# Kernel optimization log

Measured on AMD Instinct MI355X. Metric: run time of the kernel, lower is better.

## Reference

```python
import jax, jax.numpy as jnp
import numpy as np

B, S, H, D = 2, 2048, 16, 128

def setup_inputs() -> dict:
    key = jax.random.key(0)
    kq, kk, kv = jax.random.split(key, 3)
    q = jax.random.normal(kq, (B, S, H, D), dtype=jnp.float32)
    k = jax.random.normal(kk, (B, S, H, D), dtype=jnp.float32)
    v = jax.random.normal(kv, (B, S, H, D), dtype=jnp.float32)
    return {"q": q, "k": k, "v": v}

def reference(q, k, v):
    # Flash-attention semantics: layout [B, S, H, D], causal mask,
    # softmax_scale = 1/sqrt(head_dim), no dropout/window/alibi/bias.
    scale = 1.0 / jnp.sqrt(jnp.asarray(q.shape[-1], dtype=q.dtype))
    # scores: [B, H, Sq, Sk]
    scores = jnp.einsum("bqhd,bkhd->bhqk", q, k) * scale
    sq, sk = q.shape[1], k.shape[1]
    causal_mask = jnp.arange(sk)[None, :] <= jnp.arange(sq)[:, None]  # [Sq, Sk]
    scores = jnp.where(causal_mask[None, None, :, :], scores, jnp.finfo(scores.dtype).min)
    probs = jax.nn.softmax(scores, axis=-1)
    out = jnp.einsum("bhqk,bkhd->bqhd", probs, v)
    return out
```

## Files before the change

kernel.cpp:

```cpp
#include <hip/hip_runtime.h>
#include <hip/hip_bf16.h>

namespace {

constexpr int Bn = 2, Sn = 2048, Hn = 16, Dn = 128;
constexpr int QBLK = 128;
constexpr int KVBLK = 32;
constexpr int RS = Hn * Dn;
constexpr float QSCALE = 0.08838834764831845f * 1.4426950408889634f;

constexpr size_t IMG_BYTES = (size_t)Bn * Hn * 64 * 8192;
constexpr size_t WS_NEED   = 2 * IMG_BYTES;

typedef __bf16 bf16x8 __attribute__((ext_vector_type(8)));
typedef __bf16 bf16x4 __attribute__((ext_vector_type(4)));
typedef float  f32x16 __attribute__((ext_vector_type(16)));

__device__ __forceinline__ f32x16 mfma32(bf16x8 a, bf16x8 b, f32x16 c) {
  return __builtin_amdgcn_mfma_f32_32x32x16_bf16(a, b, c, 0, 0, 0);
}
__device__ __forceinline__ unsigned pack2(float a, float b) {
  union { __bf16 h[2]; unsigned u; } r;
  r.h[0] = (__bf16)a; r.h[1] = (__bf16)b;
  return r.u;
}
__device__ __forceinline__ float pair_max(float x, int hi) {
  auto r = __builtin_amdgcn_permlane32_swap(__float_as_uint(x), __float_as_uint(x), false, false);
  const float sw = __uint_as_float(hi ? r[0] : r[1]);
  return fmaxf(x, sw);
}
__device__ __forceinline__ float pair_sum(float x, int hi) {
  auto r = __builtin_amdgcn_permlane32_swap(__float_as_uint(x), __float_as_uint(x), false, false);
  const float sw = __uint_as_float(hi ? r[0] : r[1]);
  return x + sw;
}
__device__ __forceinline__ float f4e(const float4& v, int j) {
  return j == 0 ? v.x : j == 1 ? v.y : j == 2 ? v.z : v.w;
}
__device__ __forceinline__ float lane_bcast(int row, float v) {
  return __uint_as_float(__builtin_amdgcn_ds_bpermute(row * 4, __float_as_uint(v)));
}

__device__ __forceinline__ void cp16(const char* g, char* l) {
  __builtin_amdgcn_global_load_lds(
      (const __attribute__((address_space(1))) void*)g,
      (__attribute__((address_space(3))) void*)l, 16, 0, 0);
}

__device__ __forceinline__ void dma_barrier() {
  __builtin_amdgcn_sched_barrier(0);
  asm volatile("s_waitcnt vmcnt(0) lgkmcnt(0)" ::: "memory");
  __builtin_amdgcn_s_barrier();
  __builtin_amdgcn_sched_barrier(0);
}
__device__ __forceinline__ void pipeline_barrier() {
  __builtin_amdgcn_sched_barrier(0);
  asm volatile("s_waitcnt lgkmcnt(0)" ::: "memory");
  __builtin_amdgcn_s_barrier();
  __builtin_amdgcn_sched_barrier(0);
}

__global__ __launch_bounds__(256)
void prep_kv(const float* __restrict__ K, const float* __restrict__ V,
             __bf16* __restrict__ KI, __bf16* __restrict__ VI)
{
  const int gid  = (int)blockIdx.x * 256 + (int)threadIdx.x;
  const int half = gid >> 20;
  const int id   = gid & ((1 << 20) - 1);
  const int chunk = id >> 9;
  const int rem   = id & 511;
  const int bh = chunk >> 6, c = chunk & 63;
  const int b = bh >> 4, h = bh & 15;
  if (half == 0) {
    const int key = rem >> 4, dblk = rem & 15;
    const float* src = K + ((size_t)b * Sn + (size_t)c * 32 + key) * RS + h * Dn + dblk * 8;
    float4 a  = *(const float4*)src;
    float4 c2 = *(const float4*)(src + 4);
    bf16x8 f;
    f[0] = (__bf16)a.x;  f[1] = (__bf16)a.y;  f[2] = (__bf16)a.z;  f[3] = (__bf16)a.w;
    f[4] = (__bf16)c2.x; f[5] = (__bf16)c2.y; f[6] = (__bf16)c2.z; f[7] = (__bf16)c2.w;
    char* dst = (char*)KI + (size_t)chunk * 8192 + ((key * 256 + dblk * 16) ^ ((key & 7) << 4));
    *(bf16x8*)dst = f;
  } else {
    const int d = rem >> 2, koct = rem & 3;
    const float* src = V + ((size_t)b * Sn + (size_t)c * 32 + koct * 8) * RS + h * Dn + d;
    bf16x8 f;
#pragma unroll
    for (int j = 0; j < 8; ++j) f[j] = (__bf16)src[(size_t)j * RS];
    const int off = (d * 64 + koct * 16) ^ ((d & 3) << 4) ^ (((d >> 3) & 1) << 6);
    *(bf16x8*)((char*)VI + (size_t)chunk * 8192 + off) = f;
  }
}

__global__ __launch_bounds__(512)
void fa_fwd_dma(const float* __restrict__ Q, const __bf16* __restrict__ KI,
                const __bf16* __restrict__ VI, float* __restrict__ O)
{
  __shared__ __align__(16) __bf16 Klds[4][4096];
  __shared__ __align__(16) __bf16 Vt[4][4096];

  const int tid  = threadIdx.x;
  const int lane = tid & 63;
  const int wave = tid >> 6;
  const int col  = lane & 31;
  const int hi   = lane >> 5;
  const int grp  = wave >> 2;
  const int wq   = wave & 3;

  const int xcd  = (int)blockIdx.x & 7;
  const int s    = (int)blockIdx.x >> 3;
  const int hidx = xcd * 4 + (s & 3);
  const int b    = hidx >> 4, h = hidx & 15;
  const int s2   = s >> 2;
  const int qt   = (s < 32) ? (15 - s2) : (s2 - 8);
  const int q0w  = qt * QBLK + wq * 32;
  const int T    = 2 * (qt + 1);
  const size_t base = ((size_t)b * Sn) * RS + (size_t)h * Dn;

  const char* KIc = (const char*)KI + (size_t)hidx * 64 * 8192;
  const char* VIc = (const char*)VI + (size_t)hidx * 64 * 8192;

  const int sr = wave >> 1;
  const int hb = (wave & 1) * 4096;
  auto stageK2 = [&](int ss) {
    if (sr < 2) {
      const int ck = 2 * ss + sr;
      const char* g = KIc + (size_t)ck * 8192 + hb;
      char* l = (char*)&Klds[ck & 3][0] + hb;
#pragma unroll
      for (int i = 0; i < 4; ++i) cp16(g + i * 1024 + lane * 16, l + i * 1024);
    }
  };
  auto stageV2 = [&](int ss) {
    if (sr >= 2) {
      const int cv = 2 * ss + (sr - 2);
      const char* g = VIc + (size_t)cv * 8192 + hb;
      char* l = (char*)&Vt[cv & 3][0] + hb;
#pragma unroll
      for (int i = 0; i < 4; ++i) cp16(g + i * 1024 + lane * 16, l + i * 1024);
    }
  };

  const int cswz = (col & 7) << 4;
  const int vswz = ((col & 3) << 4) ^ (((col >> 3) & 1) << 6);

  bf16x8 qf[8];
  {
    const float* qp = Q + base + (size_t)(q0w + col) * RS + hi * 8;
#pragma unroll
    for (int kk = 0; kk < 8; ++kk) {
      float4 a = *(const float4*)(qp + kk * 16);
      float4 c2 = *(const float4*)(qp + kk * 16 + 4);
      bf16x8 f;
      f[0] = (__bf16)(a.x * QSCALE);  f[1] = (__bf16)(a.y * QSCALE);
      f[2] = (__bf16)(a.z * QSCALE);  f[3] = (__bf16)(a.w * QSCALE);
      f[4] = (__bf16)(c2.x * QSCALE); f[5] = (__bf16)(c2.y * QSCALE);
      f[6] = (__bf16)(c2.z * QSCALE); f[7] = (__bf16)(c2.w * QSCALE);
      qf[kk] = f;
    }
  }

  f32x16 o0 = {}, o1 = {}, o2 = {}, o3 = {};
  float m = -1e30f, l = 0.f;

  stageK2(0);
  stageV2(0);
  stageK2(1);
  dma_barrier();

  f32x16 st_cur = {};
  if (grp * KVBLK <= q0w + 31) {
    const char* kb = (const char*)&Klds[grp][0];
    __builtin_amdgcn_s_setprio(1);
#pragma unroll
    for (int kk = 0; kk < 8; ++kk) {
      bf16x8 ka = *(const bf16x8*)(kb + ((col * 256 + kk * 32 + hi * 16) ^ cswz));
      st_cur = mfma32(ka, qf[kk], st_cur);
    }
    __builtin_amdgcn_s_setprio(0);
  }
  dma_barrier();

#pragma unroll 1
  for (int t = 0; t < T; ++t) {
    if (t + 2 < T) stageK2(t + 2);
    if (t + 1 < T) stageV2(t + 1);

    f32x16 stn = {};
    const int icn = 2 * (t + 1) + grp;
    if (t + 1 < T && icn * KVBLK <= q0w + 31) {
      const char* kb = (const char*)&Klds[icn & 3][0];
      __builtin_amdgcn_s_setprio(1);
#pragma unroll
      for (int kk = 0; kk < 8; ++kk) {
        bf16x8 ka = *(const bf16x8*)(kb + ((col * 256 + kk * 32 + hi * 16) ^ cswz));
        stn = mfma32(ka, qf[kk], stn);
      }
      __builtin_amdgcn_s_setprio(0);
    }

    const int kv0 = (2 * t + grp) * KVBLK;
    if (kv0 <= q0w + 31) {
      if (kv0 + KVBLK - 1 > q0w) {
        const int qk = q0w + col - kv0;
#pragma unroll
        for (int r = 0; r < 16; ++r) {
          const int krow = (r & 3) + 8 * (r >> 2) + 4 * hi;
          st_cur[r] = (krow <= qk) ? st_cur[r] : -1e30f;
        }
      }

      float t8[8];
#pragma unroll
      for (int r = 0; r < 8; ++r) t8[r] = fmaxf(st_cur[r], st_cur[r + 8]);
#pragma unroll
      for (int r = 0; r < 4; ++r) t8[r] = fmaxf(t8[r], t8[r + 4]);
      const float pmax = pair_max(fmaxf(fmaxf(t8[0], t8[1]), fmaxf(t8[2], t8[3])), hi);

      if (!__all(pmax <= m + 11.0f)) {
        const float mnew = fmaxf(m, pmax);
        const float al = __builtin_amdgcn_exp2f(m - mnew);
        m = mnew;
        l *= al;
#pragma unroll
        for (int r = 0; r < 16; ++r) {
          const int row = (r & 3) + 8 * (r >> 2) + 4 * hi;
          const float ar = lane_bcast(row, al);
          o0[r] *= ar; o1[r] *= ar; o2[r] *= ar; o3[r] *= ar;
        }
      }

      float s4[4] = {0.f, 0.f, 0.f, 0.f};
#pragma unroll
      for (int r = 0; r < 16; ++r) {
        st_cur[r] = __builtin_amdgcn_exp2f(st_cur[r] - m);
        s4[r & 3] += st_cur[r];
      }
      l += pair_sum((s4[0] + s4[1]) + (s4[2] + s4[3]), hi);

      unsigned cw[8];
#pragma unroll
      for (int i = 0; i < 8; ++i) cw[i] = pack2(st_cur[2 * i], st_cur[2 * i + 1]);
      union { unsigned u[4]; bf16x8 v; } pa0, pa1;
      {
        auto s02 = __builtin_amdgcn_permlane32_swap(cw[0], cw[2], false, false);
        auto s13 = __builtin_amdgcn_permlane32_swap(cw[1], cw[3], false, false);
        auto s46 = __builtin_amdgcn_permlane32_swap(cw[4], cw[6], false, false);
        auto s57 = __builtin_amdgcn_permlane32_swap(cw[5], cw[7], false, false);
        pa0.u[0] = s02[0]; pa0.u[2] = s02[1];
        pa0.u[1] = s13[0]; pa0.u[3] = s13[1];
        pa1.u[0] = s46[0]; pa1.u[2] = s46[1];
        pa1.u[1] = s57[0]; pa1.u[3] = s57[1];
      }

      const char* vb = (const char*)&Vt[(2 * t + grp) & 3][0];
      __builtin_amdgcn_s_setprio(1);
#pragma unroll
      for (int ks = 0; ks < 2; ++ks) {
        const bf16x8 pa = ks ? pa1.v : pa0.v;
#define PV_STEP(ovar, dt) { \
        bf16x8 vf = *(const bf16x8*)(vb + ((((dt)*32 + col) * 64 + ks * 32 + hi * 16) ^ vswz)); \
        ovar = mfma32(pa, vf, ovar); }
        PV_STEP(o0, 0) PV_STEP(o1, 1) PV_STEP(o2, 2) PV_STEP(o3, 3)
#undef PV_STEP
      }
      __builtin_amdgcn_s_setprio(0);
    }
    dma_barrier();
    st_cur = stn;
  }

  float* ob  = reinterpret_cast<float*>(&Klds[0][0]);
  float* mlb = reinterpret_cast<float*>(&Vt[0][0]);
  if (grp == 1) {
    mlb[wq * 128 + lane] = m;
    mlb[wq * 128 + 64 + lane] = l;
#pragma unroll
    for (int r = 0; r < 16; ++r) {
      ob[wq * 1024 + r * 64 + lane] = o0[r];
      ob[4096 + wq * 1024 + r * 64 + lane] = o1[r];
    }
  }
  __syncthreads();
  float f0 = 1.f, f1 = 0.f;
  if (grp == 0) {
    const float m1 = mlb[wq * 128 + lane];
    const float l1 = mlb[wq * 128 + 64 + lane];
    const float mS = fmaxf(m, m1);
    f0 = __builtin_amdgcn_exp2f(m - mS);
    f1 = __builtin_amdgcn_exp2f(m1 - mS);
    l = l * f0 + l1 * f1;
#pragma unroll
    for (int r = 0; r < 16; ++r) {
      const int row = (r & 3) + 8 * (r >> 2) + 4 * hi;
      const float a0 = lane_bcast(row, f0), a1 = lane_bcast(row, f1);
      o0[r] = o0[r] * a0 + ob[wq * 1024 + r * 64 + lane] * a1;
      o1[r] = o1[r] * a0 + ob[4096 + wq * 1024 + r * 64 + lane] * a1;
    }
  }
  __syncthreads();
  if (grp == 1) {
#pragma unroll
    for (int r = 0; r < 16; ++r) {
      ob[wq * 1024 + r * 64 + lane] = o2[r];
      ob[4096 + wq * 1024 + r * 64 + lane] = o3[r];
    }
  }
  __syncthreads();
  if (grp == 0) {
#pragma unroll
    for (int r = 0; r < 16; ++r) {
      const int row = (r & 3) + 8 * (r >> 2) + 4 * hi;
      const float a0 = lane_bcast(row, f0), a1 = lane_bcast(row, f1);
      o2[r] = o2[r] * a0 + ob[wq * 1024 + r * 64 + lane] * a1;
      o3[r] = o3[r] * a0 + ob[4096 + wq * 1024 + r * 64 + lane] * a1;
    }
    const float linv = 1.0f / l;
#pragma unroll
    for (int r = 0; r < 16; ++r) {
      const int row = (r & 3) + 8 * (r >> 2) + 4 * hi;
      const float lr = lane_bcast(row, linv);
      float* op = O + base + (size_t)(q0w + row) * RS + col;
      op[0]  = o0[r] * lr;
      op[32] = o1[r] * lr;
      op[64] = o2[r] * lr;
      op[96] = o3[r] * lr;
    }
  }
}

__global__ __launch_bounds__(512)
void fa_fwd_reg(const float* __restrict__ Q, const float* __restrict__ K,
                const float* __restrict__ V, float* __restrict__ O)
{
  __shared__ __align__(16) __bf16 Klds[6][KVBLK * 128];
  __shared__ __align__(16) __bf16 Vt[4][128 * KVBLK];

  const int tid  = threadIdx.x;
  const int lane = tid & 63;
  const int wave = tid >> 6;
  const int col  = lane & 31;
  const int hi   = lane >> 5;
  const int grp  = wave >> 2;
  const int wq   = wave & 3;

  const int xcd  = (int)blockIdx.x & 7;
  const int s    = (int)blockIdx.x >> 3;
  const int hidx = xcd * 4 + (s & 3);
  const int b    = hidx >> 4, h = hidx & 15;
  const int s2   = s >> 2;
  const int qt   = (s < 32) ? (15 - s2) : (s2 - 8);
  const int q0w  = qt * QBLK + wq * 32;
  const int T    = 2 * (qt + 1);
  const size_t base = ((size_t)b * Sn) * RS + (size_t)h * Dn;

  const int sthalf = tid >> 8, ht = tid & 255;
  const int skey = ht >> 3, sd = (ht & 7) * 16;
  const int vkey4 = (ht & 7) * 4, vd4 = (ht >> 3) * 4;

  float4 kr[4], vr[4];
  auto loadK = [&](int ss) {
    const int kv0 = (2 * ss + sthalf) * KVBLK;
    const float* kp = K + base + (size_t)(kv0 + skey) * RS + sd;
#pragma unroll
    for (int i = 0; i < 4; ++i) kr[i] = *(const float4*)(kp + 4 * i);
  };
  auto loadV = [&](int ss) {
    const int kv0 = (2 * ss + sthalf) * KVBLK;
    const float* vp = V + base + (size_t)(kv0 + vkey4) * RS + vd4;
#pragma unroll
    for (int i = 0; i < 4; ++i) vr[i] = *(const float4*)(vp + (size_t)i * RS);
  };
  auto stageK = [&](int ss) {
    char* kb = (char*)&Klds[(2 * ss + sthalf) % 6][0];
    const int kbase = skey * 256 + sd * 2;
    const int kswz  = (skey & 7) << 4;
#pragma unroll
    for (int i = 0; i < 2; ++i) {
      bf16x8 f;
      f[0] = (__bf16)kr[2*i].x;   f[1] = (__bf16)kr[2*i].y;
      f[2] = (__bf16)kr[2*i].z;   f[3] = (__bf16)kr[2*i].w;
      f[4] = (__bf16)kr[2*i+1].x; f[5] = (__bf16)kr[2*i+1].y;
      f[6] = (__bf16)kr[2*i+1].z; f[7] = (__bf16)kr[2*i+1].w;
      *(bf16x8*)(kb + ((kbase + 16 * i) ^ kswz)) = f;
    }
  };
  auto stageV = [&](int ss) {
    char* vb = (char*)&Vt[(2 * ss + sthalf) & 3][0];
    const int b6 = ((vd4 >> 3) & 1) << 6;
#pragma unroll
    for (int j = 0; j < 4; ++j) {
      bf16x4 w;
      w[0] = (__bf16)f4e(vr[0], j);
      w[1] = (__bf16)f4e(vr[1], j);
      w[2] = (__bf16)f4e(vr[2], j);
      w[3] = (__bf16)f4e(vr[3], j);
      const int addr = (((vd4 + j) * 64 + vkey4 * 2) ^ (j << 4)) ^ b6;
      *(bf16x4*)(vb + addr) = w;
    }
  };

  const int cswz = (col & 7) << 4;
  const int vswz = ((col & 3) << 4) ^ (((col >> 3) & 1) << 6);

  bf16x8 qf[8];
  {
    const float* qp = Q + base + (size_t)(q0w + col) * RS + hi * 8;
#pragma unroll
    for (int kk = 0; kk < 8; ++kk) {
      float4 a = *(const float4*)(qp + kk * 16);
      float4 c2 = *(const float4*)(qp + kk * 16 + 4);
      bf16x8 f;
      f[0] = (__bf16)(a.x * QSCALE);  f[1] = (__bf16)(a.y * QSCALE);
      f[2] = (__bf16)(a.z * QSCALE);  f[3] = (__bf16)(a.w * QSCALE);
      f[4] = (__bf16)(c2.x * QSCALE); f[5] = (__bf16)(c2.y * QSCALE);
      f[6] = (__bf16)(c2.z * QSCALE); f[7] = (__bf16)(c2.w * QSCALE);
      qf[kk] = f;
    }
  }

  f32x16 o0 = {}, o1 = {}, o2 = {}, o3 = {};
  float m = -1e30f, l = 0.f;

  loadK(0); loadV(0);
  stageK(0);
  loadK(1);
  stageV(0);
  loadV(1);
  stageK(1);
  if (2 < T) loadK(2);
  pipeline_barrier();

  f32x16 st_cur = {};
  if (grp * KVBLK <= q0w + 31) {
    const char* kb = (const char*)&Klds[grp][0];
    __builtin_amdgcn_s_setprio(1);
#pragma unroll
    for (int kk = 0; kk < 8; ++kk) {
      bf16x8 ka = *(const bf16x8*)(kb + ((col * 256 + kk * 32 + hi * 16) ^ cswz));
      st_cur = mfma32(ka, qf[kk], st_cur);
    }
    __builtin_amdgcn_s_setprio(0);
  }

#pragma unroll 1
  for (int t = 0; t < T; ++t) {
    f32x16 stn = {};
    const int icn = 2 * (t + 1) + grp;
    if (t + 1 < T && icn * KVBLK <= q0w + 31) {
      const char* kb = (const char*)&Klds[icn % 6][0];
      __builtin_amdgcn_s_setprio(1);
#pragma unroll
      for (int kk = 0; kk < 8; ++kk) {
        bf16x8 ka = *(const bf16x8*)(kb + ((col * 256 + kk * 32 + hi * 16) ^ cswz));
        stn = mfma32(ka, qf[kk], stn);
      }
      __builtin_amdgcn_s_setprio(0);
    }

    if (t + 2 < T) stageK(t + 2);
    if (t + 1 < T) stageV(t + 1);
    if (t + 3 < T) loadK(t + 3);
    if (t + 2 < T) loadV(t + 2);

    const int kv0 = (2 * t + grp) * KVBLK;
    if (kv0 <= q0w + 31) {
      if (kv0 + KVBLK - 1 > q0w) {
        const int qk = q0w + col - kv0;
#pragma unroll
        for (int r = 0; r < 16; ++r) {
          const int krow = (r & 3) + 8 * (r >> 2) + 4 * hi;
          st_cur[r] = (krow <= qk) ? st_cur[r] : -1e30f;
        }
      }

      float t8[8];
#pragma unroll
      for (int r = 0; r < 8; ++r) t8[r] = fmaxf(st_cur[r], st_cur[r + 8]);
#pragma unroll
      for (int r = 0; r < 4; ++r) t8[r] = fmaxf(t8[r], t8[r + 4]);
      const float pmax = pair_max(fmaxf(fmaxf(t8[0], t8[1]), fmaxf(t8[2], t8[3])), hi);

      if (!__all(pmax <= m + 11.0f)) {
        const float mnew = fmaxf(m, pmax);
        const float al = __builtin_amdgcn_exp2f(m - mnew);
        m = mnew;
        l *= al;
#pragma unroll
        for (int r = 0; r < 16; ++r) {
          const int row = (r & 3) + 8 * (r >> 2) + 4 * hi;
          const float ar = lane_bcast(row, al);
          o0[r] *= ar; o1[r] *= ar; o2[r] *= ar; o3[r] *= ar;
        }
      }

      float s4[4] = {0.f, 0.f, 0.f, 0.f};
#pragma unroll
      for (int r = 0; r < 16; ++r) {
        st_cur[r] = __builtin_amdgcn_exp2f(st_cur[r] - m);
        s4[r & 3] += st_cur[r];
      }
      l += pair_sum((s4[0] + s4[1]) + (s4[2] + s4[3]), hi);

      unsigned cw[8];
#pragma unroll
      for (int i = 0; i < 8; ++i) cw[i] = pack2(st_cur[2 * i], st_cur[2 * i + 1]);
      union { unsigned u[4]; bf16x8 v; } pa0, pa1;
      {
        auto s02 = __builtin_amdgcn_permlane32_swap(cw[0], cw[2], false, false);
        auto s13 = __builtin_amdgcn_permlane32_swap(cw[1], cw[3], false, false);
        auto s46 = __builtin_amdgcn_permlane32_swap(cw[4], cw[6], false, false);
        auto s57 = __builtin_amdgcn_permlane32_swap(cw[5], cw[7], false, false);
        pa0.u[0] = s02[0]; pa0.u[2] = s02[1];
        pa0.u[1] = s13[0]; pa0.u[3] = s13[1];
        pa1.u[0] = s46[0]; pa1.u[2] = s46[1];
        pa1.u[1] = s57[0]; pa1.u[3] = s57[1];
      }

      const char* vb = (const char*)&Vt[(2 * t + grp) & 3][0];
      __builtin_amdgcn_s_setprio(1);
#pragma unroll
      for (int ks = 0; ks < 2; ++ks) {
        const bf16x8 pa = ks ? pa1.v : pa0.v;
#define PV_STEP(ovar, dt) { \
        bf16x8 vf = *(const bf16x8*)(vb + ((((dt)*32 + col) * 64 + ks * 32 + hi * 16) ^ vswz)); \
        ovar = mfma32(pa, vf, ovar); }
        PV_STEP(o0, 0) PV_STEP(o1, 1) PV_STEP(o2, 2) PV_STEP(o3, 3)
#undef PV_STEP
      }
      __builtin_amdgcn_s_setprio(0);
    }
    pipeline_barrier();
    st_cur = stn;
  }

  float* ob  = reinterpret_cast<float*>(&Klds[0][0]);
  float* mlb = reinterpret_cast<float*>(&Vt[0][0]);
  if (grp == 1) {
    mlb[wq * 128 + lane] = m;
    mlb[wq * 128 + 64 + lane] = l;
#pragma unroll
    for (int r = 0; r < 16; ++r) {
      ob[wq * 1024 + r * 64 + lane] = o0[r];
      ob[4096 + wq * 1024 + r * 64 + lane] = o1[r];
    }
  }
  __syncthreads();
  float f0 = 1.f, f1 = 0.f;
  if (grp == 0) {
    const float m1 = mlb[wq * 128 + lane];
    const float l1 = mlb[wq * 128 + 64 + lane];
    const float mS = fmaxf(m, m1);
    f0 = __builtin_amdgcn_exp2f(m - mS);
    f1 = __builtin_amdgcn_exp2f(m1 - mS);
    l = l * f0 + l1 * f1;
#pragma unroll
    for (int r = 0; r < 16; ++r) {
      const int row = (r & 3) + 8 * (r >> 2) + 4 * hi;
      const float a0 = lane_bcast(row, f0), a1 = lane_bcast(row, f1);
      o0[r] = o0[r] * a0 + ob[wq * 1024 + r * 64 + lane] * a1;
      o1[r] = o1[r] * a0 + ob[4096 + wq * 1024 + r * 64 + lane] * a1;
    }
  }
  __syncthreads();
  if (grp == 1) {
#pragma unroll
    for (int r = 0; r < 16; ++r) {
      ob[wq * 1024 + r * 64 + lane] = o2[r];
      ob[4096 + wq * 1024 + r * 64 + lane] = o3[r];
    }
  }
  __syncthreads();
  if (grp == 0) {
#pragma unroll
    for (int r = 0; r < 16; ++r) {
      const int row = (r & 3) + 8 * (r >> 2) + 4 * hi;
      const float a0 = lane_bcast(row, f0), a1 = lane_bcast(row, f1);
      o2[r] = o2[r] * a0 + ob[wq * 1024 + r * 64 + lane] * a1;
      o3[r] = o3[r] * a0 + ob[4096 + wq * 1024 + r * 64 + lane] * a1;
    }
    const float linv = 1.0f / l;
#pragma unroll
    for (int r = 0; r < 16; ++r) {
      const int row = (r & 3) + 8 * (r >> 2) + 4 * hi;
      const float lr = lane_bcast(row, linv);
      float* op = O + base + (size_t)(q0w + row) * RS + col;
      op[0]  = o0[r] * lr;
      op[32] = o1[r] * lr;
      op[64] = o2[r] * lr;
      op[96] = o3[r] * lr;
    }
  }
}

}

extern "C" void kernel_launch(void* const* d_in, const int* , int ,
                              void* d_out, int , void* d_ws, size_t ws_size,
                              hipStream_t stream) {
  const float* q = (const float*)d_in[0];
  const float* k = (const float*)d_in[1];
  const float* v = (const float*)d_in[2];
  float* o = (float*)d_out;
  if (d_ws != nullptr && ws_size >= WS_NEED) {
    __bf16* ki = (__bf16*)d_ws;
    __bf16* vi = (__bf16*)((char*)d_ws + IMG_BYTES);
    hipLaunchKernelGGL(prep_kv, dim3(8192), dim3(256), 0, stream, k, v, ki, vi);
    hipLaunchKernelGGL(fa_fwd_dma, dim3(512), dim3(512), 0, stream, q, ki, vi, o);
  } else {
    hipLaunchKernelGGL(fa_fwd_reg, dim3(512), dim3(512), 0, stream, q, k, v, o);
  }
}
```

Measured before the change: 102.3 us.

## Pair causal q-tiles per block and widen KV steps to 64 keys

Each block now handles two complementary query tiles (15-p and p) in sequence, halving the grid to 256 blocks so causal work is balanced per block. Each wave group now processes two 32-key chunks per iteration using an 8-deep LDS ring for K and V, which halves the number of barriers per key. The cost is double the shared memory (128 KB) and more live score registers, which may reduce occupancy. It also serialises two tiles inside one block, so there is less parallelism across CUs.

```diff
diff --git a/kernel.cpp b/kernel.cpp
--- a/kernel.cpp
+++ b/kernel.cpp
@@ -96,8 +96,295 @@
 void fa_fwd_dma(const float* __restrict__ Q, const __bf16* __restrict__ KI,
                 const __bf16* __restrict__ VI, float* __restrict__ O)
 {
-  __shared__ __align__(16) __bf16 Klds[4][4096];
-  __shared__ __align__(16) __bf16 Vt[4][4096];
+  __shared__ __align__(16) __bf16 Klds[8][4096];
+  __shared__ __align__(16) __bf16 Vt[8][4096];
+
+  const int tid  = threadIdx.x;
+  const int lane = tid & 63;
+  const int wave = tid >> 6;
+  const int col  = lane & 31;
+  const int hi   = lane >> 5;
+  const int grp  = wave >> 2;
+  const int wq   = wave & 3;
+
+  const int xcd  = (int)blockIdx.x & 7;
+  const int s    = (int)blockIdx.x >> 3;
+  const int hidx = xcd * 4 + (s & 3);
+  const int b    = hidx >> 4, h = hidx & 15;
+  const int p    = s >> 2;
+  const size_t base = ((size_t)b * Sn) * RS + (size_t)h * Dn;
+
+  const char* KIc = (const char*)KI + (size_t)hidx * 64 * 8192;
+  const char* VIc = (const char*)VI + (size_t)hidx * 64 * 8192;
+
+  auto stageKc = [&](int cc) {
+    const char* g = KIc + (size_t)cc * 8192 + lane * 16;
+    char* l = (char*)&Klds[cc & 7][0];
+#pragma unroll
+    for (int i = 0; i < 8; ++i) cp16(g + i * 1024, l + i * 1024);
+  };
+  auto stageVc = [&](int cc) {
+    const char* g = VIc + (size_t)cc * 8192 + lane * 16;
+    char* l = (char*)&Vt[cc & 7][0];
+#pragma unroll
+    for (int i = 0; i < 8; ++i) cp16(g + i * 1024, l + i * 1024);
+  };
+
+  const int cswz = (col & 7) << 4;
+  const int vswz = ((col & 3) << 4) ^ (((col >> 3) & 1) << 6);
+
+#define QK8(kbp, acc) { \
+  __builtin_amdgcn_s_setprio(1); \
+  _Pragma("unroll") \
+  for (int kk = 0; kk < 8; ++kk) { \
+    bf16x8 ka = *(const bf16x8*)((kbp) + ((col * 256 + kk * 32 + hi * 16) ^ cswz)); \
+    acc = mfma32(ka, qf[kk], acc); \
+  } \
+  __builtin_amdgcn_s_setprio(0); }
+
+#pragma unroll 1
+  for (int tp = 0; tp < 2; ++tp) {
+    const int qt  = tp ? p : (15 - p);
+    const int q0w = qt * QBLK + wq * 32;
+    const int T   = qt + 1;
+
+    bf16x8 qf[8];
+    {
+      const float* qp = Q + base + (size_t)(q0w + col) * RS + hi * 8;
+#pragma unroll
+      for (int kk = 0; kk < 8; ++kk) {
+        float4 a = *(const float4*)(qp + kk * 16);
+        float4 c2 = *(const float4*)(qp + kk * 16 + 4);
+        bf16x8 f;
+        f[0] = (__bf16)(a.x * QSCALE);  f[1] = (__bf16)(a.y * QSCALE);
+        f[2] = (__bf16)(a.z * QSCALE);  f[3] = (__bf16)(a.w * QSCALE);
+        f[4] = (__bf16)(c2.x * QSCALE); f[5] = (__bf16)(c2.y * QSCALE);
+        f[6] = (__bf16)(c2.z * QSCALE); f[7] = (__bf16)(c2.w * QSCALE);
+        qf[kk] = f;
+      }
+    }
+
+    f32x16 o0 = {}, o1 = {}, o2 = {}, o3 = {};
+    float m = -1e30f, l = 0.f;
+
+    if (wave < 4) stageKc(wave); else stageVc(wave - 4);
+    if (T > 1 && wave < 4) stageKc(4 + wave);
+    dma_barrier();
+
+    f32x16 sc0 = {}, sc1 = {};
+    {
+      const int cc = 2 * grp;
+      if (cc * 32 <= q0w + 31) {
+        const char* kb = (const char*)&Klds[cc][0];
+        QK8(kb, sc0)
+        if ((cc + 1) * 32 <= q0w + 31) {
+          const char* kb1 = (const char*)&Klds[cc + 1][0];
+          QK8(kb1, sc1)
+        }
+      }
+    }
+    dma_barrier();
+
+#pragma unroll 1
+    for (int t = 0; t < T; ++t) {
+      if (t + 2 < T && wave < 4) stageKc(4 * (t + 2) + wave);
+      if (t + 1 < T && wave >= 4) stageVc(4 * (t + 1) + (wave - 4));
+
+      f32x16 sn0 = {}, sn1 = {};
+      if (t + 1 < T) {
+        const int cc = 4 * (t + 1) + 2 * grp;
+        if (cc * 32 <= q0w + 31) {
+          const char* kb = (const char*)&Klds[cc & 7][0];
+          QK8(kb, sn0)
+          if ((cc + 1) * 32 <= q0w + 31) {
+            const char* kb1 = (const char*)&Klds[(cc + 1) & 7][0];
+            QK8(kb1, sn1)
+          }
+        }
+      }
+
+      const int cc0 = 4 * t + 2 * grp;
+      const int kv0 = cc0 * 32;
+      if (kv0 <= q0w + 31) {
+        const bool v1 = (kv0 + 32) <= q0w + 31;
+
+        if (kv0 + 31 > q0w) {
+          const int qk = q0w + col - kv0;
+#pragma unroll
+          for (int r = 0; r < 16; ++r) {
+            const int krow = (r & 3) + 8 * (r >> 2) + 4 * hi;
+            sc0[r] = (krow <= qk) ? sc0[r] : -1e30f;
+          }
+        }
+        if (v1 && kv0 + 63 > q0w) {
+          const int qk1 = q0w + col - (kv0 + 32);
+#pragma unroll
+          for (int r = 0; r < 16; ++r) {
+            const int krow = (r & 3) + 8 * (r >> 2) + 4 * hi;
+            sc1[r] = (krow <= qk1) ? sc1[r] : -1e30f;
+          }
+        }
+
+        float t8[8];
+#pragma unroll
+        for (int r = 0; r < 8; ++r) t8[r] = fmaxf(sc0[r], sc0[r + 8]);
+        if (v1) {
+#pragma unroll
+          for (int r = 0; r < 8; ++r) t8[r] = fmaxf(t8[r], fmaxf(sc1[r], sc1[r + 8]));
+        }
+#pragma unroll
+        for (int r = 0; r < 4; ++r) t8[r] = fmaxf(t8[r], t8[r + 4]);
+        const float pmax = pair_max(fmaxf(fmaxf(t8[0], t8[1]), fmaxf(t8[2], t8[3])), hi);
+
+        if (!__all(pmax <= m + 11.0f)) {
+          const float mnew = fmaxf(m, pmax);
+          const float al = __builtin_amdgcn_exp2f(m - mnew);
+          m = mnew;
+          l *= al;
+#pragma unroll
+          for (int r = 0; r < 16; ++r) {
+            const int row = (r & 3) + 8 * (r >> 2) + 4 * hi;
+            const float ar = lane_bcast(row, al);
+            o0[r] *= ar; o1[r] *= ar; o2[r] *= ar; o3[r] *= ar;
+          }
+        }
+
+        float s4[4] = {0.f, 0.f, 0.f, 0.f};
+#pragma unroll
+        for (int r = 0; r < 16; ++r) {
+          sc0[r] = __builtin_amdgcn_exp2f(sc0[r] - m);
+          s4[r & 3] += sc0[r];
+        }
+        if (v1) {
+#pragma unroll
+          for (int r = 0; r < 16; ++r) {
+            sc1[r] = __builtin_amdgcn_exp2f(sc1[r] - m);
+            s4[r & 3] += sc1[r];
+          }
+        }
+        l += pair_sum((s4[0] + s4[1]) + (s4[2] + s4[3]), hi);
+
+        union { unsigned u[4]; bf16x8 v; } pa0, pa1, pb0, pb1;
+        {
+          unsigned cw[8];
+#pragma unroll
+          for (int i = 0; i < 8; ++i) cw[i] = pack2(sc0[2 * i], sc0[2 * i + 1]);
+          auto s02 = __builtin_amdgcn_permlane32_swap(cw[0], cw[2], false, false);
+          auto s13 = __builtin_amdgcn_permlane32_swap(cw[1], cw[3], false, false);
+          auto s46 = __builtin_amdgcn_permlane32_swap(cw[4], cw[6], false, false);
+          auto s57 = __builtin_amdgcn_permlane32_swap(cw[5], cw[7], false, false);
+          pa0.u[0] = s02[0]; pa0.u[2] = s02[1];
+          pa0.u[1] = s13[0]; pa0.u[3] = s13[1];
+          pa1.u[0] = s46[0]; pa1.u[2] = s46[1];
+          pa1.u[1] = s57[0]; pa1.u[3] = s57[1];
+        }
+        if (v1) {
+          unsigned cw[8];
+#pragma unroll
+          for (int i = 0; i < 8; ++i) cw[i] = pack2(sc1[2 * i], sc1[2 * i + 1]);
+          auto s02 = __builtin_amdgcn_permlane32_swap(cw[0], cw[2], false, false);
+          auto s13 = __builtin_amdgcn_permlane32_swap(cw[1], cw[3], false, false);
+          auto s46 = __builtin_amdgcn_permlane32_swap(cw[4], cw[6], false, false);
+          auto s57 = __builtin_amdgcn_permlane32_swap(cw[5], cw[7], false, false);
+          pb0.u[0] = s02[0]; pb0.u[2] = s02[1];
+          pb0.u[1] = s13[0]; pb0.u[3] = s13[1];
+          pb1.u[0] = s46[0]; pb1.u[2] = s46[1];
+          pb1.u[1] = s57[0]; pb1.u[3] = s57[1];
+        }
+
+        const char* vb0 = (const char*)&Vt[cc0 & 7][0];
+        const char* vb1 = (const char*)&Vt[(cc0 + 1) & 7][0];
+        __builtin_amdgcn_s_setprio(1);
+#pragma unroll
+        for (int ks = 0; ks < 2; ++ks) {
+          const bf16x8 pa = ks ? pa1.v : pa0.v;
+#define PV_STEP(ovar, dt, vbp) { \
+          bf16x8 vf = *(const bf16x8*)((vbp) + ((((dt)*32 + col) * 64 + ks * 32 + hi * 16) ^ vswz)); \
+          ovar = mfma32(pa, vf, ovar); }
+          PV_STEP(o0, 0, vb0) PV_STEP(o1, 1, vb0) PV_STEP(o2, 2, vb0) PV_STEP(o3, 3, vb0)
+        }
+        if (v1) {
+#pragma unroll
+          for (int ks = 0; ks < 2; ++ks) {
+            const bf16x8 pa = ks ? pb1.v : pb0.v;
+            PV_STEP(o0, 0, vb1) PV_STEP(o1, 1, vb1) PV_STEP(o2, 2, vb1) PV_STEP(o3, 3, vb1)
+#undef PV_STEP
+          }
+        }
+        __builtin_amdgcn_s_setprio(0);
+      }
+      dma_barrier();
+      sc0 = sn0; sc1 = sn1;
+    }
+
+    float* ob  = reinterpret_cast<float*>(&Klds[0][0]);
+    float* mlb = reinterpret_cast<float*>(&Vt[0][0]);
+    if (grp == 1) {
+      mlb[wq * 128 + lane] = m;
+      mlb[wq * 128 + 64 + lane] = l;
+#pragma unroll
+      for (int r = 0; r < 16; ++r) {
+        ob[wq * 1024 + r * 64 + lane] = o0[r];
+        ob[4096 + wq * 1024 + r * 64 + lane] = o1[r];
+      }
+    }
+    __syncthreads();
+    float f0 = 1.f, f1 = 0.f;
+    if (grp == 0) {
+      const float m1 = mlb[wq * 128 + lane];
+      const float l1 = mlb[wq * 128 + 64 + lane];
+      const float mS = fmaxf(m, m1);
+      f0 = __builtin_amdgcn_exp2f(m - mS);
+      f1 = __builtin_amdgcn_exp2f(m1 - mS);
+      l = l * f0 + l1 * f1;
+#pragma unroll
+      for (int r = 0; r < 16; ++r) {
+        const int row = (r & 3) + 8 * (r >> 2) + 4 * hi;
+        const float a0 = lane_bcast(row, f0), a1 = lane_bcast(row, f1);
+        o0[r] = o0[r] * a0 + ob[wq * 1024 + r * 64 + lane] * a1;
+        o1[r] = o1[r] * a0 + ob[4096 + wq * 1024 + r * 64 + lane] * a1;
+      }
+    }
+    __syncthreads();
+    if (grp == 1) {
+#pragma unroll
+      for (int r = 0; r < 16; ++r) {
+        ob[wq * 1024 + r * 64 + lane] = o2[r];
+        ob[4096 + wq * 1024 + r * 64 + lane] = o3[r];
+      }
+    }
+    __syncthreads();
+    if (grp == 0) {
+#pragma unroll
+      for (int r = 0; r < 16; ++r) {
+        const int row = (r & 3) + 8 * (r >> 2) + 4 * hi;
+        const float a0 = lane_bcast(row, f0), a1 = lane_bcast(row, f1);
+        o2[r] = o2[r] * a0 + ob[wq * 1024 + r * 64 + lane] * a1;
+        o3[r] = o3[r] * a0 + ob[4096 + wq * 1024 + r * 64 + lane] * a1;
+      }
+      const float linv = 1.0f / l;
+#pragma unroll
+      for (int r = 0; r < 16; ++r) {
+        const int row = (r & 3) + 8 * (r >> 2) + 4 * hi;
+        const float lr = lane_bcast(row, linv);
+        float* op = O + base + (size_t)(q0w + row) * RS + col;
+        op[0]  = o0[r] * lr;
+        op[32] = o1[r] * lr;
+        op[64] = o2[r] * lr;
+        op[96] = o3[r] * lr;
+      }
+    }
+    __syncthreads();
+  }
+#undef QK8
+}
+
+__global__ __launch_bounds__(512)
+void fa_fwd_reg(const float* __restrict__ Q, const float* __restrict__ K,
+                const float* __restrict__ V, float* __restrict__ O)
+{
+  __shared__ __align__(16) __bf16 Klds[6][KVBLK * 128];
+  __shared__ __align__(16) __bf16 Vt[4][128 * KVBLK];
 
   const int tid  = threadIdx.x;
   const int lane = tid & 63;
@@ -117,27 +404,49 @@
   const int T    = 2 * (qt + 1);
   const size_t base = ((size_t)b * Sn) * RS + (size_t)h * Dn;
 
-  const char* KIc = (const char*)KI + (size_t)hidx * 64 * 8192;
-  const char* VIc = (const char*)VI + (size_t)hidx * 64 * 8192;
-
-  const int sr = wave >> 1;
-  const int hb = (wave & 1) * 4096;
-  auto stageK2 = [&](int ss) {
-    if (sr < 2) {
-      const int ck = 2 * ss + sr;
-      const char* g = KIc + (size_t)ck * 8192 + hb;
-      char* l = (char*)&Klds[ck & 3][0] + hb;
-#pragma unroll
-      for (int i = 0; i < 4; ++i) cp16(g + i * 1024 + lane * 16, l + i * 1024);
-    }
+  const int sthalf = tid >> 8, ht = tid & 255;
+  const int skey = ht >> 3, sd = (ht & 7) * 16;
+  const int vkey4 = (ht & 7) * 4, vd4 = (ht >> 3) * 4;
+
+  float4 kr[4], vr[4];
+  auto loadK = [&](int ss) {
+    const int kv0 = (2 * ss + sthalf) * KVBLK;
+    const float* kp = K + base + (size_t)(kv0 + skey) * RS + sd;
+#pragma unroll
+    for (int i = 0; i < 4; ++i) kr[i] = *(const float4*)(kp + 4 * i);
   };
-  auto stageV2 = [&](int ss) {
-    if (sr >= 2) {
-      const int cv = 2 * ss + (sr - 2);
-      const char* g = VIc + (size_t)cv * 8192 + hb;
-      char* l = (char*)&Vt[cv & 3][0] + hb;
-#pragma unroll
-      for (int i = 0; i < 4; ++i) cp16(g + i * 1024 + lane * 16, l + i * 1024);
+  auto loadV = [&](int ss) {
+    const int kv0 = (2 * ss + sthalf) * KVBLK;
+    const float* vp = V + base + (size_t)(kv0 + vkey4) * RS + vd4;
+#pragma unroll
+    for (int i = 0; i < 4; ++i) vr[i] = *(const float4*)(vp + (size_t)i * RS);
+  };
+  auto stageK = [&](int ss) {
+    char* kb = (char*)&Klds[(2 * ss + sthalf) % 6][0];
+    const int kbase = skey * 256 + sd * 2;
+    const int kswz  = (skey & 7) << 4;
+#pragma unroll
+    for (int i = 0; i < 2; ++i) {
+      bf16x8 f;
+      f[0] = (__bf16)kr[2*i].x;   f[1] = (__bf16)kr[2*i].y;
+      f[2] = (__bf16)kr[2*i].z;   f[3] = (__bf16)kr[2*i].w;
+      f[4] = (__bf16)kr[2*i+1].x; f[5] = (__bf16)kr[2*i+1].y;
+      f[6] = (__bf16)kr[2*i+1].z; f[7] = (__bf16)kr[2*i+1].w;
+      *(bf16x8*)(kb + ((kbase + 16 * i) ^ kswz)) = f;
+    }
+  };
+  auto stageV = [&](int ss) {
+    char* vb = (char*)&Vt[(2 * ss + sthalf) & 3][0];
+    const int b6 = ((vd4 >> 3) & 1) << 6;
+#pragma unroll
+    for (int j = 0; j < 4; ++j) {
+      bf16x4 w;
+      w[0] = (__bf16)f4e(vr[0], j);
+      w[1] = (__bf16)f4e(vr[1], j);
+      w[2] = (__bf16)f4e(vr[2], j);
+      w[3] = (__bf16)f4e(vr[3], j);
+      const int addr = (((vd4 + j) * 64 + vkey4 * 2) ^ (j << 4)) ^ b6;
+      *(bf16x4*)(vb + addr) = w;
     }
   };
 
@@ -163,10 +472,14 @@
   f32x16 o0 = {}, o1 = {}, o2 = {}, o3 = {};
   float m = -1e30f, l = 0.f;
 
-  stageK2(0);
-  stageV2(0);
-  stageK2(1);
-  dma_barrier();
+  loadK(0); loadV(0);
+  stageK(0);
+  loadK(1);
+  stageV(0);
+  loadV(1);
+  stageK(1);
+  if (2 < T) loadK(2);
+  pipeline_barrier();
 
   f32x16 st_cur = {};
   if (grp * KVBLK <= q0w + 31) {
@@ -179,17 +492,13 @@
     }
     __builtin_amdgcn_s_setprio(0);
   }
-  dma_barrier();
 
 #pragma unroll 1
   for (int t = 0; t < T; ++t) {
-    if (t + 2 < T) stageK2(t + 2);
-    if (t + 1 < T) stageV2(t + 1);
-
     f32x16 stn = {};
     const int icn = 2 * (t + 1) + grp;
     if (t + 1 < T && icn * KVBLK <= q0w + 31) {
-      const char* kb = (const char*)&Klds[icn & 3][0];
+      const char* kb = (const char*)&Klds[icn % 6][0];
       __builtin_amdgcn_s_setprio(1);
 #pragma unroll
       for (int kk = 0; kk < 8; ++kk) {
@@ -198,6 +507,11 @@
       }
       __builtin_amdgcn_s_setprio(0);
     }
+
+    if (t + 2 < T) stageK(t + 2);
+    if (t + 1 < T) stageV(t + 1);
+    if (t + 3 < T) loadK(t + 3);
+    if (t + 2 < T) loadV(t + 2);
 
     const int kv0 = (2 * t + grp) * KVBLK;
     if (kv0 <= q0w + 31) {
@@ -266,270 +580,6 @@
       }
       __builtin_amdgcn_s_setprio(0);
     }
-    dma_barrier();
-    st_cur = stn;
-  }
-
-  float* ob  = reinterpret_cast<float*>(&Klds[0][0]);
-  float* mlb = reinterpret_cast<float*>(&Vt[0][0]);
-  if (grp == 1) {
-    mlb[wq * 128 + lane] = m;
-    mlb[wq * 128 + 64 + lane] = l;
-#pragma unroll
-    for (int r = 0; r < 16; ++r) {
-      ob[wq * 1024 + r * 64 + lane] = o0[r];
-      ob[4096 + wq * 1024 + r * 64 + lane] = o1[r];
-    }
-  }
-  __syncthreads();
-  float f0 = 1.f, f1 = 0.f;
-  if (grp == 0) {
-    const float m1 = mlb[wq * 128 + lane];
-    const float l1 = mlb[wq * 128 + 64 + lane];
-    const float mS = fmaxf(m, m1);
-    f0 = __builtin_amdgcn_exp2f(m - mS);
-    f1 = __builtin_amdgcn_exp2f(m1 - mS);
-    l = l * f0 + l1 * f1;
-#pragma unroll
-    for (int r = 0; r < 16; ++r) {
-      const int row = (r & 3) + 8 * (r >> 2) + 4 * hi;
-      const float a0 = lane_bcast(row, f0), a1 = lane_bcast(row, f1);
-      o0[r] = o0[r] * a0 + ob[wq * 1024 + r * 64 + lane] * a1;
-      o1[r] = o1[r] * a0 + ob[4096 + wq * 1024 + r * 64 + lane] * a1;
-    }
-  }
-  __syncthreads();
-  if (grp == 1) {
-#pragma unroll
-    for (int r = 0; r < 16; ++r) {
-      ob[wq * 1024 + r * 64 + lane] = o2[r];
-      ob[4096 + wq * 1024 + r * 64 + lane] = o3[r];
-    }
-  }
-  __syncthreads();
-  if (grp == 0) {
-#pragma unroll
-    for (int r = 0; r < 16; ++r) {
-      const int row = (r & 3) + 8 * (r >> 2) + 4 * hi;
-      const float a0 = lane_bcast(row, f0), a1 = lane_bcast(row, f1);
-      o2[r] = o2[r] * a0 + ob[wq * 1024 + r * 64 + lane] * a1;
-      o3[r] = o3[r] * a0 + ob[4096 + wq * 1024 + r * 64 + lane] * a1;
-    }
-    const float linv = 1.0f / l;
-#pragma unroll
-    for (int r = 0; r < 16; ++r) {
-      const int row = (r & 3) + 8 * (r >> 2) + 4 * hi;
-      const float lr = lane_bcast(row, linv);
-      float* op = O + base + (size_t)(q0w + row) * RS + col;
-      op[0]  = o0[r] * lr;
-      op[32] = o1[r] * lr;
-      op[64] = o2[r] * lr;
-      op[96] = o3[r] * lr;
-    }
-  }
-}
-
-__global__ __launch_bounds__(512)
-void fa_fwd_reg(const float* __restrict__ Q, const float* __restrict__ K,
-                const float* __restrict__ V, float* __restrict__ O)
-{
-  __shared__ __align__(16) __bf16 Klds[6][KVBLK * 128];
-  __shared__ __align__(16) __bf16 Vt[4][128 * KVBLK];
-
-  const int tid  = threadIdx.x;
-  const int lane = tid & 63;
-  const int wave = tid >> 6;
-  const int col  = lane & 31;
-  const int hi   = lane >> 5;
-  const int grp  = wave >> 2;
-  const int wq   = wave & 3;
-
-  const int xcd  = (int)blockIdx.x & 7;
-  const int s    = (int)blockIdx.x >> 3;
-  const int hidx = xcd * 4 + (s & 3);
-  const int b    = hidx >> 4, h = hidx & 15;
-  const int s2   = s >> 2;
-  const int qt   = (s < 32) ? (15 - s2) : (s2 - 8);
-  const int q0w  = qt * QBLK + wq * 32;
-  const int T    = 2 * (qt + 1);
-  const size_t base = ((size_t)b * Sn) * RS + (size_t)h * Dn;
-
-  const int sthalf = tid >> 8, ht = tid & 255;
-  const int skey = ht >> 3, sd = (ht & 7) * 16;
-  const int vkey4 = (ht & 7) * 4, vd4 = (ht >> 3) * 4;
-
-  float4 kr[4], vr[4];
-  auto loadK = [&](int ss) {
-    const int kv0 = (2 * ss + sthalf) * KVBLK;
-    const float* kp = K + base + (size_t)(kv0 + skey) * RS + sd;
-#pragma unroll
-    for (int i = 0; i < 4; ++i) kr[i] = *(const float4*)(kp + 4 * i);
-  };
-  auto loadV = [&](int ss) {
-    const int kv0 = (2 * ss + sthalf) * KVBLK;
-    const float* vp = V + base + (size_t)(kv0 + vkey4) * RS + vd4;
-#pragma unroll
-    for (int i = 0; i < 4; ++i) vr[i] = *(const float4*)(vp + (size_t)i * RS);
-  };
-  auto stageK = [&](int ss) {
-    char* kb = (char*)&Klds[(2 * ss + sthalf) % 6][0];
-    const int kbase = skey * 256 + sd * 2;
-    const int kswz  = (skey & 7) << 4;
-#pragma unroll
-    for (int i = 0; i < 2; ++i) {
-      bf16x8 f;
-      f[0] = (__bf16)kr[2*i].x;   f[1] = (__bf16)kr[2*i].y;
-      f[2] = (__bf16)kr[2*i].z;   f[3] = (__bf16)kr[2*i].w;
-      f[4] = (__bf16)kr[2*i+1].x; f[5] = (__bf16)kr[2*i+1].y;
-      f[6] = (__bf16)kr[2*i+1].z; f[7] = (__bf16)kr[2*i+1].w;
-      *(bf16x8*)(kb + ((kbase + 16 * i) ^ kswz)) = f;
-    }
-  };
-  auto stageV = [&](int ss) {
-    char* vb = (char*)&Vt[(2 * ss + sthalf) & 3][0];
-    const int b6 = ((vd4 >> 3) & 1) << 6;
-#pragma unroll
-    for (int j = 0; j < 4; ++j) {
-      bf16x4 w;
-      w[0] = (__bf16)f4e(vr[0], j);
-      w[1] = (__bf16)f4e(vr[1], j);
-      w[2] = (__bf16)f4e(vr[2], j);
-      w[3] = (__bf16)f4e(vr[3], j);
-      const int addr = (((vd4 + j) * 64 + vkey4 * 2) ^ (j << 4)) ^ b6;
-      *(bf16x4*)(vb + addr) = w;
-    }
-  };
-
-  const int cswz = (col & 7) << 4;
-  const int vswz = ((col & 3) << 4) ^ (((col >> 3) & 1) << 6);
-
-  bf16x8 qf[8];
-  {
-    const float* qp = Q + base + (size_t)(q0w + col) * RS + hi * 8;
-#pragma unroll
-    for (int kk = 0; kk < 8; ++kk) {
-      float4 a = *(const float4*)(qp + kk * 16);
-      float4 c2 = *(const float4*)(qp + kk * 16 + 4);
-      bf16x8 f;
-      f[0] = (__bf16)(a.x * QSCALE);  f[1] = (__bf16)(a.y * QSCALE);
-      f[2] = (__bf16)(a.z * QSCALE);  f[3] = (__bf16)(a.w * QSCALE);
-      f[4] = (__bf16)(c2.x * QSCALE); f[5] = (__bf16)(c2.y * QSCALE);
-      f[6] = (__bf16)(c2.z * QSCALE); f[7] = (__bf16)(c2.w * QSCALE);
-      qf[kk] = f;
-    }
-  }
-
-  f32x16 o0 = {}, o1 = {}, o2 = {}, o3 = {};
-  float m = -1e30f, l = 0.f;
-
-  loadK(0); loadV(0);
-  stageK(0);
-  loadK(1);
-  stageV(0);
-  loadV(1);
-  stageK(1);
-  if (2 < T) loadK(2);
-  pipeline_barrier();
-
-  f32x16 st_cur = {};
-  if (grp * KVBLK <= q0w + 31) {
-    const char* kb = (const char*)&Klds[grp][0];
-    __builtin_amdgcn_s_setprio(1);
-#pragma unroll
-    for (int kk = 0; kk < 8; ++kk) {
-      bf16x8 ka = *(const bf16x8*)(kb + ((col * 256 + kk * 32 + hi * 16) ^ cswz));
-      st_cur = mfma32(ka, qf[kk], st_cur);
-    }
-    __builtin_amdgcn_s_setprio(0);
-  }
-
-#pragma unroll 1
-  for (int t = 0; t < T; ++t) {
-    f32x16 stn = {};
-    const int icn = 2 * (t + 1) + grp;
-    if (t + 1 < T && icn * KVBLK <= q0w + 31) {
-      const char* kb = (const char*)&Klds[icn % 6][0];
-      __builtin_amdgcn_s_setprio(1);
-#pragma unroll
-      for (int kk = 0; kk < 8; ++kk) {
-        bf16x8 ka = *(const bf16x8*)(kb + ((col * 256 + kk * 32 + hi * 16) ^ cswz));
-        stn = mfma32(ka, qf[kk], stn);
-      }
-      __builtin_amdgcn_s_setprio(0);
-    }
-
-    if (t + 2 < T) stageK(t + 2);
-    if (t + 1 < T) stageV(t + 1);
-    if (t + 3 < T) loadK(t + 3);
-    if (t + 2 < T) loadV(t + 2);
-
-    const int kv0 = (2 * t + grp) * KVBLK;
-    if (kv0 <= q0w + 31) {
-      if (kv0 + KVBLK - 1 > q0w) {
-        const int qk = q0w + col - kv0;
-#pragma unroll
-        for (int r = 0; r < 16; ++r) {
-          const int krow = (r & 3) + 8 * (r >> 2) + 4 * hi;
-          st_cur[r] = (krow <= qk) ? st_cur[r] : -1e30f;
-        }
-      }
-
-      float t8[8];
-#pragma unroll
-      for (int r = 0; r < 8; ++r) t8[r] = fmaxf(st_cur[r], st_cur[r + 8]);
-#pragma unroll
-      for (int r = 0; r < 4; ++r) t8[r] = fmaxf(t8[r], t8[r + 4]);
-      const float pmax = pair_max(fmaxf(fmaxf(t8[0], t8[1]), fmaxf(t8[2], t8[3])), hi);
-
-      if (!__all(pmax <= m + 11.0f)) {
-        const float mnew = fmaxf(m, pmax);
-        const float al = __builtin_amdgcn_exp2f(m - mnew);
-        m = mnew;
-        l *= al;
-#pragma unroll
-        for (int r = 0; r < 16; ++r) {
-          const int row = (r & 3) + 8 * (r >> 2) + 4 * hi;
-          const float ar = lane_bcast(row, al);
-          o0[r] *= ar; o1[r] *= ar; o2[r] *= ar; o3[r] *= ar;
-        }
-      }
-
-      float s4[4] = {0.f, 0.f, 0.f, 0.f};
-#pragma unroll
-      for (int r = 0; r < 16; ++r) {
-        st_cur[r] = __builtin_amdgcn_exp2f(st_cur[r] - m);
-        s4[r & 3] += st_cur[r];
-      }
-      l += pair_sum((s4[0] + s4[1]) + (s4[2] + s4[3]), hi);
-
-      unsigned cw[8];
-#pragma unroll
-      for (int i = 0; i < 8; ++i) cw[i] = pack2(st_cur[2 * i], st_cur[2 * i + 1]);
-      union { unsigned u[4]; bf16x8 v; } pa0, pa1;
-      {
-        auto s02 = __builtin_amdgcn_permlane32_swap(cw[0], cw[2], false, false);
-        auto s13 = __builtin_amdgcn_permlane32_swap(cw[1], cw[3], false, false);
-        auto s46 = __builtin_amdgcn_permlane32_swap(cw[4], cw[6], false, false);
-        auto s57 = __builtin_amdgcn_permlane32_swap(cw[5], cw[7], false, false);
-        pa0.u[0] = s02[0]; pa0.u[2] = s02[1];
-        pa0.u[1] = s13[0]; pa0.u[3] = s13[1];
-        pa1.u[0] = s46[0]; pa1.u[2] = s46[1];
-        pa1.u[1] = s57[0]; pa1.u[3] = s57[1];
-      }
-
-      const char* vb = (const char*)&Vt[(2 * t + grp) & 3][0];
-      __builtin_amdgcn_s_setprio(1);
-#pragma unroll
-      for (int ks = 0; ks < 2; ++ks) {
-        const bf16x8 pa = ks ? pa1.v : pa0.v;
-#define PV_STEP(ovar, dt) { \
-        bf16x8 vf = *(const bf16x8*)(vb + ((((dt)*32 + col) * 64 + ks * 32 + hi * 16) ^ vswz)); \
-        ovar = mfma32(pa, vf, ovar); }
-        PV_STEP(o0, 0) PV_STEP(o1, 1) PV_STEP(o2, 2) PV_STEP(o3, 3)
-#undef PV_STEP
-      }
-      __builtin_amdgcn_s_setprio(0);
-    }
     pipeline_barrier();
     st_cur = stn;
   }
@@ -606,7 +656,7 @@
     __bf16* ki = (__bf16*)d_ws;
     __bf16* vi = (__bf16*)((char*)d_ws + IMG_BYTES);
     hipLaunchKernelGGL(prep_kv, dim3(8192), dim3(256), 0, stream, k, v, ki, vi);
-    hipLaunchKernelGGL(fa_fwd_dma, dim3(512), dim3(512), 0, stream, q, ki, vi, o);
+    hipLaunchKernelGGL(fa_fwd_dma, dim3(256), dim3(512), 0, stream, q, ki, vi, o);
   } else {
     hipLaunchKernelGGL(fa_fwd_reg, dim3(512), dim3(512), 0, stream, q, k, v, o);
   }
```

Measured after the change: 97.30 us. 4.9% less time.
